# Optimization experiments

Hardware: AMD Instinct MI355X
Metric: run time of the kernel (lower is better)

## Reference

```python
import jax, jax.numpy as jnp
import numpy as np

NS = 100000
H = 128  # embedding_dim
K = 4    # heads


def setup_inputs() -> dict:
    key = jax.random.key(0)
    ks = jax.random.split(key, 8)
    return {
        "e": jax.random.normal(ks[0], (NS, H), dtype=jnp.float32),
        "w_key": jax.random.normal(ks[1], (K, 1), dtype=jnp.float32),
        "w_value": jax.random.normal(ks[2], (K, 1), dtype=jnp.float32),
        "q": jax.random.normal(ks[3], (H,), dtype=jnp.float32),
        "mu_w": jax.random.normal(ks[4], (1, H), dtype=jnp.float32) * (1.0 / np.sqrt(H)),
        "mu_b": jax.random.normal(ks[5], (1,), dtype=jnp.float32) * 0.01,
        "sigma_w": jax.random.normal(ks[6], (1, H), dtype=jnp.float32) * (1.0 / np.sqrt(H)),
        "sigma_b": jax.random.normal(ks[7], (1,), dtype=jnp.float32) * 0.01,
    }


def reference(e, w_key, w_value, q, mu_w, mu_b, sigma_w, sigma_b):
    # e: [Ns, H] -> unsqueeze(0) -> [1, Ns, H]
    e3 = e[None, :, :]
    # w_key/w_value: [K, 1]; einsum 'kd,dnh->knh' -> [K, Ns, H]
    k = jnp.einsum('kd,dnh->knh', w_key, e3)
    v = jnp.einsum('kd,dnh->knh', w_value, e3)
    # L2-normalized attention logits: [K, Ns]
    q_norm = jnp.linalg.norm(q)                    # scalar
    k_norm = jnp.linalg.norm(k, axis=-1)           # [K, Ns]
    a_att = jnp.einsum('h,knh->kn', q, k) / (q_norm * k_norm)
    a_att = jnp.maximum(a_att, 0.0)
    a_att = a_att / jnp.maximum(jnp.sum(a_att, axis=-1, keepdims=True), 1e-6)
    # weighted aggregation over stocks: [K, H]
    h_multi = jnp.einsum('kn,knh->kh', a_att, v)
    # linear heads -> [K]
    mu_z = jnp.squeeze(h_multi @ mu_w.T + mu_b, axis=-1)
    sigma_z = jax.nn.softplus(jnp.squeeze(h_multi @ sigma_w.T + sigma_b, axis=-1))
    return (mu_z, sigma_z)
```

## Files before the change

kernel.cpp:

```cpp
#include <hip/hip_runtime.h>
#include <math.h>

#define NS 100000
#define H 128
#define NHEADS 4
#define TPB 256
#define NBLK 3125
#define NREP 32

__device__ __forceinline__ float dot4(float4 a, float4 b) {
    return a.x * b.x + a.y * b.y + a.z * b.z + a.w * b.w;
}

__device__ __forceinline__ void fma4(float4& acc, float w, float4 v) {
    acc.x = fmaf(w, v.x, acc.x); acc.y = fmaf(w, v.y, acc.y);
    acc.z = fmaf(w, v.z, acc.z); acc.w = fmaf(w, v.w, acc.w);
}

__global__ __launch_bounds__(TPB, 8) void fp_pass1(const float* __restrict__ e,
                                                   const float* __restrict__ q,
                                                   float* __restrict__ g) {
    const int tid  = threadIdx.x;
    const int lane = tid & 63;
    const int widx = tid >> 6;
    const int half = lane >> 5;
    const int c4   = (lane & 31) << 2;

    const int gw = blockIdx.x * (TPB / 64) + widx;
    const float* p = e + (size_t)gw * (8 * H) + (size_t)half * H + c4;
    const float4 v0 = *(const float4*)(p);
    const float4 v1 = *(const float4*)(p + 2 * H);
    const float4 v2 = *(const float4*)(p + 4 * H);
    const float4 v3 = *(const float4*)(p + 6 * H);

    const float4 q4 = *(const float4*)(q + c4);
    float qn = dot4(q4, q4);
    qn += __shfl_xor(qn, 1);  qn += __shfl_xor(qn, 2);  qn += __shfl_xor(qn, 4);
    qn += __shfl_xor(qn, 8);  qn += __shfl_xor(qn, 16);
    const float inv_qn = rsqrtf(qn);

    float d0 = dot4(v0, q4), d1 = dot4(v1, q4), d2 = dot4(v2, q4), d3 = dot4(v3, q4);
    float s0 = dot4(v0, v0), s1 = dot4(v1, v1), s2 = dot4(v2, v2), s3 = dot4(v3, v3);
#define LVL(m)                                                        \
    d0 += __shfl_xor(d0, m); d1 += __shfl_xor(d1, m);                 \
    d2 += __shfl_xor(d2, m); d3 += __shfl_xor(d3, m);                 \
    s0 += __shfl_xor(s0, m); s1 += __shfl_xor(s1, m);                 \
    s2 += __shfl_xor(s2, m); s3 += __shfl_xor(s3, m);
    LVL(1) LVL(2) LVL(4) LVL(8) LVL(16)
#undef LVL
    const float c0 = d0 * rsqrtf(s0) * inv_qn;
    const float c1 = d1 * rsqrtf(s1) * inv_qn;
    const float c2 = d2 * rsqrtf(s2) * inv_qn;
    const float c3 = d3 * rsqrtf(s3) * inv_qn;
    const float wp0 = fmaxf(c0, 0.f), wm0 = fmaxf(-c0, 0.f);
    const float wp1 = fmaxf(c1, 0.f), wm1 = fmaxf(-c1, 0.f);
    const float wp2 = fmaxf(c2, 0.f), wm2 = fmaxf(-c2, 0.f);
    const float wp3 = fmaxf(c3, 0.f), wm3 = fmaxf(-c3, 0.f);
    const float sp = (wp0 + wp1) + (wp2 + wp3);
    const float sm = (wm0 + wm1) + (wm2 + wm3);
    float4 up = {0.f, 0.f, 0.f, 0.f};
    float4 um = {0.f, 0.f, 0.f, 0.f};
    fma4(up, wp0, v0); fma4(up, wp1, v1); fma4(up, wp2, v2); fma4(up, wp3, v3);
    fma4(um, wm0, v0); fma4(um, wm1, v1); fma4(um, wm2, v2); fma4(um, wm3, v3);

    __shared__ float s_up[8][H];
    __shared__ float s_um[8][H];
    __shared__ float s_s[8][2];
    const int hs = widx * 2 + half;
    *(float4*)(&s_up[hs][c4]) = up;
    *(float4*)(&s_um[hs][c4]) = um;
    if ((lane & 31) == 0) {
        s_s[hs][0] = sp;
        s_s[hs][1] = sm;
    }
    __syncthreads();

    float* gr = g + (blockIdx.x & (NREP - 1)) * 258;
    if (tid < H) {
        float a = 0.f;
#pragma unroll
        for (int h2 = 0; h2 < 8; ++h2) a += s_up[h2][tid];
        atomicAdd(&gr[tid], a);
    } else {
        const int t = tid - H;
        float a = 0.f;
#pragma unroll
        for (int h2 = 0; h2 < 8; ++h2) a += s_um[h2][t];
        atomicAdd(&gr[H + t], a);
    }
    if (tid < 2) {
        float a = 0.f;
#pragma unroll
        for (int h2 = 0; h2 < 8; ++h2) a += s_s[h2][tid];
        atomicAdd(&gr[256 + tid], a);
    }
}

__global__ __launch_bounds__(256) void fp_finalize(const float* __restrict__ g,
                                                   const float* __restrict__ w_key,
                                                   const float* __restrict__ w_value,
                                                   const float* __restrict__ mu_w,
                                                   const float* __restrict__ mu_b,
                                                   const float* __restrict__ sigma_w,
                                                   const float* __restrict__ sigma_b,
                                                   float* __restrict__ out) {
    __shared__ float tot[258];
    const int tid = threadIdx.x;
    {
        float a = 0.f;
#pragma unroll
        for (int r = 0; r < NREP; ++r) a += g[r * 258 + tid];
        tot[tid] = a;
    }
    if (tid < 2) {
        float a = 0.f;
#pragma unroll
        for (int r = 0; r < NREP; ++r) a += g[r * 258 + 256 + tid];
        tot[256 + tid] = a;
    }
    __syncthreads();

    if (tid < 64) {
        const int l = tid;
        const float up0 = tot[2 * l], up1 = tot[2 * l + 1];
        const float um0 = tot[H + 2 * l], um1 = tot[H + 2 * l + 1];
        const float mw0 = mu_w[2 * l], mw1 = mu_w[2 * l + 1];
        const float sw0 = sigma_w[2 * l], sw1 = sigma_w[2 * l + 1];
        float A = up0 * mw0 + up1 * mw1;
        float B = up0 * sw0 + up1 * sw1;
        float C = um0 * mw0 + um1 * mw1;
        float D = um0 * sw0 + um1 * sw1;
#pragma unroll
        for (int m = 1; m < 64; m <<= 1) {
            A += __shfl_xor(A, m);
            B += __shfl_xor(B, m);
            C += __shfl_xor(C, m);
            D += __shfl_xor(D, m);
        }
        if (l < NHEADS) {
            const float spv = fmaxf(tot[256], 1e-6f);
            const float smv = fmaxf(tot[257], 1e-6f);
            const float wk = w_key[l];
            const float wv = w_value[l];
            float dmu, dsg;
            if (wk > 0.f) {
                dmu = A / spv; dsg = B / spv;
            } else if (wk < 0.f) {
                dmu = C / smv; dsg = D / smv;
            } else {
                dmu = 0.f; dsg = 0.f;
            }
            out[l] = fmaf(wv, dmu, mu_b[0]);
            const float x = fmaf(wv, dsg, sigma_b[0]);
            out[NHEADS + l] = fmaxf(x, 0.f) + log1pf(expf(-fabsf(x)));
        }
    }
}

extern "C" void kernel_launch(void* const* d_in, const int* in_sizes, int n_in,
                              void* d_out, int out_size, void* d_ws, size_t ws_size,
                              hipStream_t stream) {
    const float* e       = (const float*)d_in[0];
    const float* w_key   = (const float*)d_in[1];
    const float* w_value = (const float*)d_in[2];
    const float* q       = (const float*)d_in[3];
    const float* mu_w    = (const float*)d_in[4];
    const float* mu_b    = (const float*)d_in[5];
    const float* sigma_w = (const float*)d_in[6];
    const float* sigma_b = (const float*)d_in[7];
    float* out = (float*)d_out;
    float* g   = (float*)d_ws;

    hipLaunchKernelGGL(fp_pass1, dim3(NBLK), dim3(TPB), 0, stream, e, q, g);
    hipLaunchKernelGGL(fp_finalize, dim3(1), dim3(256), 0, stream, g,
                       w_key, w_value, mu_w, mu_b, sigma_w, sigma_b, out);
}
```

Baseline: 98.42 us.

## Replace atomic partial accumulation with per-block rows and two-stage reduction

Each block of the main pass now writes its partial sums to a dedicated row instead of atomically adding into 32 replicated rows. A new 32-block reduce kernel folds the per-block rows into 32 rows, which the finalize kernel then sums. This removes atomic contention and the dependence on a pre-zeroed workspace. In exchange it adds a kernel launch and extra global traffic for roughly 3 MB of partials, read by a small grid.

```diff
diff --git a/kernel.cpp b/kernel.cpp
--- a/kernel.cpp
+++ b/kernel.cpp
@@ -6,7 +6,9 @@
 #define NHEADS 4
 #define TPB 256
 #define NBLK 3125
-#define NREP 32
+#define ROWSTRIDE 258
+#define NR2 32
+#define ROWS_PER ((NBLK + NR2 - 1) / NR2)
 
 __device__ __forceinline__ float dot4(float4 a, float4 b) {
     return a.x * b.x + a.y * b.y + a.z * b.z + a.w * b.w;
@@ -19,7 +21,7 @@
 
 __global__ __launch_bounds__(TPB, 8) void fp_pass1(const float* __restrict__ e,
                                                    const float* __restrict__ q,
-                                                   float* __restrict__ g) {
+                                                   float* __restrict__ partial) {
     const int tid  = threadIdx.x;
     const int lane = tid & 63;
     const int widx = tid >> 6;
@@ -75,28 +77,43 @@
     }
     __syncthreads();
 
-    float* gr = g + (blockIdx.x & (NREP - 1)) * 258;
+    float* row = partial + (size_t)blockIdx.x * ROWSTRIDE;
+    float a = 0.f;
     if (tid < H) {
-        float a = 0.f;
 #pragma unroll
         for (int h2 = 0; h2 < 8; ++h2) a += s_up[h2][tid];
-        atomicAdd(&gr[tid], a);
+        row[tid] = a;
     } else {
         const int t = tid - H;
-        float a = 0.f;
 #pragma unroll
         for (int h2 = 0; h2 < 8; ++h2) a += s_um[h2][t];
-        atomicAdd(&gr[H + t], a);
+        row[H + t] = a;
     }
     if (tid < 2) {
-        float a = 0.f;
+        float b2 = 0.f;
 #pragma unroll
-        for (int h2 = 0; h2 < 8; ++h2) a += s_s[h2][tid];
-        atomicAdd(&gr[256 + tid], a);
+        for (int h2 = 0; h2 < 8; ++h2) b2 += s_s[h2][tid];
+        row[256 + tid] = b2;
     }
 }
 
-__global__ __launch_bounds__(256) void fp_finalize(const float* __restrict__ g,
+__global__ __launch_bounds__(256) void fp_reduce(const float* __restrict__ partial,
+                                                 float* __restrict__ out2) {
+    const int tid = threadIdx.x;
+    const int r0 = blockIdx.x * ROWS_PER;
+    const int r1 = min(r0 + ROWS_PER, NBLK);
+    float a = 0.f, b = 0.f;
+    for (int r = r0; r < r1; ++r) {
+        const float* row = partial + (size_t)r * ROWSTRIDE;
+        a += row[tid];
+        if (tid < 2) b += row[256 + tid];
+    }
+    float* orow = out2 + (size_t)blockIdx.x * ROWSTRIDE;
+    orow[tid] = a;
+    if (tid < 2) orow[256 + tid] = b;
+}
+
+__global__ __launch_bounds__(256) void fp_finalize(const float* __restrict__ out2,
                                                    const float* __restrict__ w_key,
                                                    const float* __restrict__ w_value,
                                                    const float* __restrict__ mu_w,
@@ -104,18 +121,18 @@
                                                    const float* __restrict__ sigma_w,
                                                    const float* __restrict__ sigma_b,
                                                    float* __restrict__ out) {
-    __shared__ float tot[258];
+    __shared__ float tot[ROWSTRIDE];
     const int tid = threadIdx.x;
     {
         float a = 0.f;
 #pragma unroll
-        for (int r = 0; r < NREP; ++r) a += g[r * 258 + tid];
+        for (int r = 0; r < NR2; ++r) a += out2[r * ROWSTRIDE + tid];
         tot[tid] = a;
     }
     if (tid < 2) {
         float a = 0.f;
 #pragma unroll
-        for (int r = 0; r < NREP; ++r) a += g[r * 258 + 256 + tid];
+        for (int r = 0; r < NR2; ++r) a += out2[r * ROWSTRIDE + 256 + tid];
         tot[256 + tid] = a;
     }
     __syncthreads();
@@ -168,10 +185,12 @@
     const float* mu_b    = (const float*)d_in[5];
     const float* sigma_w = (const float*)d_in[6];
     const float* sigma_b = (const float*)d_in[7];
-    float* out = (float*)d_out;
-    float* g   = (float*)d_ws;
+    float* out     = (float*)d_out;
+    float* partial = (float*)d_ws;
+    float* out2    = partial + (size_t)NBLK * ROWSTRIDE;
 
-    hipLaunchKernelGGL(fp_pass1, dim3(NBLK), dim3(TPB), 0, stream, e, q, g);
-    hipLaunchKernelGGL(fp_finalize, dim3(1), dim3(256), 0, stream, g,
+    hipLaunchKernelGGL(fp_pass1, dim3(NBLK), dim3(TPB), 0, stream, e, q, partial);
+    hipLaunchKernelGGL(fp_reduce, dim3(NR2), dim3(256), 0, stream, partial, out2);
+    hipLaunchKernelGGL(fp_finalize, dim3(1), dim3(256), 0, stream, out2,
                        w_key, w_value, mu_w, mu_b, sigma_w, sigma_b, out);
 }
```

Result: slower. 124.8 us (+26.8%).

## Project block partial sums onto mu/sigma weights before atomics to cut atomic traffic

Applied to the files above, without the earlier changes.

Each block now dots its summed positive and negative weighted vectors with mu_w and sigma_w in-block. It then atomically adds only six scalars, padded to separate cache lines and spread over 64 replica slots, instead of 258 floats per block. The finalize kernel shrinks to summing six values and applying the heads. This targets atomic contention and traffic in the memory-bound pass, at the cost of an extra block barrier and wave reductions in every block.

```diff
diff --git a/kernel.cpp b/kernel.cpp
--- a/kernel.cpp
+++ b/kernel.cpp
@@ -6,7 +6,8 @@
 #define NHEADS 4
 #define TPB 256
 #define NBLK 3125
-#define NREP 32
+#define NREP 64
+#define SLOTF 16
 
 __device__ __forceinline__ float dot4(float4 a, float4 b) {
     return a.x * b.x + a.y * b.y + a.z * b.z + a.w * b.w;
@@ -19,6 +20,8 @@
 
 __global__ __launch_bounds__(TPB, 8) void fp_pass1(const float* __restrict__ e,
                                                    const float* __restrict__ q,
+                                                   const float* __restrict__ mu_w,
+                                                   const float* __restrict__ sigma_w,
                                                    float* __restrict__ g) {
     const int tid  = threadIdx.x;
     const int lane = tid & 63;
@@ -75,85 +78,76 @@
     }
     __syncthreads();
 
-    float* gr = g + (blockIdx.x & (NREP - 1)) * 258;
+    const int col = tid & (H - 1);
+    float a = 0.f;
     if (tid < H) {
-        float a = 0.f;
 #pragma unroll
-        for (int h2 = 0; h2 < 8; ++h2) a += s_up[h2][tid];
-        atomicAdd(&gr[tid], a);
+        for (int h2 = 0; h2 < 8; ++h2) a += s_up[h2][col];
     } else {
-        const int t = tid - H;
-        float a = 0.f;
 #pragma unroll
-        for (int h2 = 0; h2 < 8; ++h2) a += s_um[h2][t];
-        atomicAdd(&gr[H + t], a);
+        for (int h2 = 0; h2 < 8; ++h2) a += s_um[h2][col];
     }
-    if (tid < 2) {
-        float a = 0.f;
+    float pA = a * mu_w[col];
+    float pB = a * sigma_w[col];
 #pragma unroll
-        for (int h2 = 0; h2 < 8; ++h2) a += s_s[h2][tid];
-        atomicAdd(&gr[256 + tid], a);
+    for (int m = 1; m < 64; m <<= 1) {
+        pA += __shfl_xor(pA, m);
+        pB += __shfl_xor(pB, m);
+    }
+    __shared__ float s_r[4][2];
+    if (lane == 0) { s_r[widx][0] = pA; s_r[widx][1] = pB; }
+    __syncthreads();
+
+    if (tid == 0) {
+        const float A = s_r[0][0] + s_r[1][0];
+        const float B = s_r[0][1] + s_r[1][1];
+        const float C = s_r[2][0] + s_r[3][0];
+        const float D = s_r[2][1] + s_r[3][1];
+        float spv = 0.f, smv = 0.f;
+#pragma unroll
+        for (int h2 = 0; h2 < 8; ++h2) { spv += s_s[h2][0]; smv += s_s[h2][1]; }
+        float* slot = g + (size_t)(blockIdx.x & (NREP - 1)) * 6 * SLOTF;
+        atomicAdd(slot + 0 * SLOTF, A);
+        atomicAdd(slot + 1 * SLOTF, B);
+        atomicAdd(slot + 2 * SLOTF, C);
+        atomicAdd(slot + 3 * SLOTF, D);
+        atomicAdd(slot + 4 * SLOTF, spv);
+        atomicAdd(slot + 5 * SLOTF, smv);
     }
 }
 
-__global__ __launch_bounds__(256) void fp_finalize(const float* __restrict__ g,
-                                                   const float* __restrict__ w_key,
-                                                   const float* __restrict__ w_value,
-                                                   const float* __restrict__ mu_w,
-                                                   const float* __restrict__ mu_b,
-                                                   const float* __restrict__ sigma_w,
-                                                   const float* __restrict__ sigma_b,
-                                                   float* __restrict__ out) {
-    __shared__ float tot[258];
+__global__ __launch_bounds__(64) void fp_finalize(const float* __restrict__ g,
+                                                  const float* __restrict__ w_key,
+                                                  const float* __restrict__ w_value,
+                                                  const float* __restrict__ mu_b,
+                                                  const float* __restrict__ sigma_b,
+                                                  float* __restrict__ out) {
     const int tid = threadIdx.x;
-    {
+    __shared__ float tot[6];
+    if (tid < 6) {
         float a = 0.f;
 #pragma unroll
-        for (int r = 0; r < NREP; ++r) a += g[r * 258 + tid];
+        for (int r = 0; r < NREP; ++r) a += g[(size_t)(r * 6 + tid) * SLOTF];
         tot[tid] = a;
     }
-    if (tid < 2) {
-        float a = 0.f;
-#pragma unroll
-        for (int r = 0; r < NREP; ++r) a += g[r * 258 + 256 + tid];
-        tot[256 + tid] = a;
-    }
     __syncthreads();
-
-    if (tid < 64) {
-        const int l = tid;
-        const float up0 = tot[2 * l], up1 = tot[2 * l + 1];
-        const float um0 = tot[H + 2 * l], um1 = tot[H + 2 * l + 1];
-        const float mw0 = mu_w[2 * l], mw1 = mu_w[2 * l + 1];
-        const float sw0 = sigma_w[2 * l], sw1 = sigma_w[2 * l + 1];
-        float A = up0 * mw0 + up1 * mw1;
-        float B = up0 * sw0 + up1 * sw1;
-        float C = um0 * mw0 + um1 * mw1;
-        float D = um0 * sw0 + um1 * sw1;
-#pragma unroll
-        for (int m = 1; m < 64; m <<= 1) {
-            A += __shfl_xor(A, m);
-            B += __shfl_xor(B, m);
-            C += __shfl_xor(C, m);
-            D += __shfl_xor(D, m);
+    if (tid < NHEADS) {
+        const float A = tot[0], B = tot[1], C = tot[2], D = tot[3];
+        const float spv = fmaxf(tot[4], 1e-6f);
+        const float smv = fmaxf(tot[5], 1e-6f);
+        const float wk = w_key[tid];
+        const float wv = w_value[tid];
+        float dmu, dsg;
+        if (wk > 0.f) {
+            dmu = A / spv; dsg = B / spv;
+        } else if (wk < 0.f) {
+            dmu = C / smv; dsg = D / smv;
+        } else {
+            dmu = 0.f; dsg = 0.f;
         }
-        if (l < NHEADS) {
-            const float spv = fmaxf(tot[256], 1e-6f);
-            const float smv = fmaxf(tot[257], 1e-6f);
-            const float wk = w_key[l];
-            const float wv = w_value[l];
-            float dmu, dsg;
-            if (wk > 0.f) {
-                dmu = A / spv; dsg = B / spv;
-            } else if (wk < 0.f) {
-                dmu = C / smv; dsg = D / smv;
-            } else {
-                dmu = 0.f; dsg = 0.f;
-            }
-            out[l] = fmaf(wv, dmu, mu_b[0]);
-            const float x = fmaf(wv, dsg, sigma_b[0]);
-            out[NHEADS + l] = fmaxf(x, 0.f) + log1pf(expf(-fabsf(x)));
-        }
+        out[tid] = fmaf(wv, dmu, mu_b[0]);
+        const float x = fmaf(wv, dsg, sigma_b[0]);
+        out[NHEADS + tid] = fmaxf(x, 0.f) + log1pf(expf(-fabsf(x)));
     }
 }
 
@@ -171,7 +165,8 @@
     float* out = (float*)d_out;
     float* g   = (float*)d_ws;
 
-    hipLaunchKernelGGL(fp_pass1, dim3(NBLK), dim3(TPB), 0, stream, e, q, g);
-    hipLaunchKernelGGL(fp_finalize, dim3(1), dim3(256), 0, stream, g,
-                       w_key, w_value, mu_w, mu_b, sigma_w, sigma_b, out);
+    hipLaunchKernelGGL(fp_pass1, dim3(NBLK), dim3(TPB), 0, stream,
+                       e, q, mu_w, sigma_w, g);
+    hipLaunchKernelGGL(fp_finalize, dim3(1), dim3(64), 0, stream, g,
+                       w_key, w_value, mu_b, sigma_b, out);
 }
```

Result: no change. 99.34 us (+0.9%).
